# Kernel optimization log

Hardware: AMD Instinct MI355X
Metric: run time of the kernel (lower is better)

Reference implementation:

```python
import jax, jax.numpy as jnp
import numpy as np


def _rel_coords_log(ws: int) -> np.ndarray:
    # matches torch.meshgrid default indexing='ij'
    idx = np.arange(ws, dtype=np.float32)
    coords = np.stack(np.meshgrid(idx, idx, indexing='ij'), axis=0).reshape(2, -1)  # [2, ws^2]
    rel = coords[:, :, None] - coords[:, None, :]  # [2, T, T]
    rel = rel.transpose(1, 2, 0).reshape(-1, 2)    # [T*T, 2]
    return np.sign(rel) * np.log1p(np.abs(rel))


def setup_inputs() -> dict:
    key = jax.random.key(0)
    ks = jax.random.split(key, 9)
    B, C, Hd, ws, meta_h = 256, 256, 8, 16, 256
    s = 1.0 / np.sqrt(C)
    return {
        'x': jax.random.normal(ks[0], (B, C, ws, ws), dtype=jnp.float32),
        'w_qkv': jax.random.normal(ks[1], (3 * C, C), dtype=jnp.float32) * s,
        'b_qkv': jax.random.normal(ks[2], (3 * C,), dtype=jnp.float32) * 0.01,
        'w_proj': jax.random.normal(ks[3], (C, C), dtype=jnp.float32) * s,
        'b_proj': jax.random.normal(ks[4], (C,), dtype=jnp.float32) * 0.01,
        'mw1': jax.random.normal(ks[5], (meta_h, 2), dtype=jnp.float32) * 0.5,
        'mb1': jax.random.normal(ks[6], (meta_h,), dtype=jnp.float32) * 0.01,
        'mw2': jax.random.normal(ks[7], (Hd, meta_h), dtype=jnp.float32) * (1.0 / np.sqrt(meta_h)),
        'mb2': jax.random.normal(ks[8], (Hd,), dtype=jnp.float32) * 0.01,
        'tau': jnp.ones((1, Hd, 1, 1), dtype=jnp.float32),
    }


def reference(x, w_qkv, b_qkv, w_proj, b_proj, mw1, mb1, mw2, mb2, tau):
    B, C, H, W = x.shape
    T = H * W
    nh = tau.shape[1]
    hd = C // nh
    # [B, C, H, W] -> [B, T, C]
    xt = x.reshape(B, C, T).transpose(0, 2, 1)
    qkv = xt @ w_qkv.T + b_qkv                                  # [B, T, 3C]
    qkv = qkv.reshape(B, T, 3, nh, hd).transpose(2, 0, 3, 1, 4)  # [3, B, nh, T, hd]
    q, k, v = qkv[0], qkv[1], qkv[2]
    # cosine similarity attention
    qn = jnp.linalg.norm(q, axis=-1, keepdims=True)              # [B, nh, T, 1]
    kn = jnp.linalg.norm(k, axis=-1, keepdims=True)
    denom = jnp.maximum(qn * kn.transpose(0, 1, 3, 2), 1e-6)
    scores = jnp.einsum('bhqd,bhkd->bhqk', q, k) / denom
    scores = scores / jnp.maximum(tau, 0.01)
    # MLP relative position bias (static coords)
    rc = jnp.asarray(_rel_coords_log(H))                          # [T*T, 2]
    bias = jax.nn.relu(rc @ mw1.T + mb1) @ mw2.T + mb2            # [T*T, nh]
    bias = bias.T.reshape(nh, T, T)
    scores = scores + bias[None]
    attn = jax.nn.softmax(scores, axis=-1)
    out = jnp.einsum('bhqk,bhkd->bhqd', attn, v)                  # [B, nh, T, hd]
    out = out.transpose(0, 2, 1, 3).reshape(B, T, C)
    out = out @ w_proj.T + b_proj
    return out.transpose(0, 2, 1).reshape(B, C, H, W)
```

## Files before the change

kernel.cpp:

```cpp
#include <hip/hip_runtime.h>
#include <math.h>

#define Cc 256
#define NH 8
#define HD 32
#define Tt 256
#define MH 256
#define TBL 961

typedef _Float16 f16;
typedef f16 f16x4 __attribute__((ext_vector_type(4)));
typedef f16 f16x8 __attribute__((ext_vector_type(8)));
typedef float f32x4 __attribute__((ext_vector_type(4)));

__device__ __forceinline__ f16x8 ld8(const f16* base, int row, int kc) {
  return *(const f16x8*)&base[row * 32 + ((kc ^ ((row >> 2) & 3)) << 3)];
}
__device__ __forceinline__ void st8(f16* base, int row, int kc, f16x8 v) {
  *(f16x8*)&base[row * 32 + ((kc ^ ((row >> 2) & 3)) << 3)] = v;
}
__device__ __forceinline__ int sidx(int row, int col) {
  return row * 32 + (((col >> 3) ^ ((row >> 2) & 3)) << 3) + (col & 7);
}
__device__ __forceinline__ int vsidx(int d, int t) {
  return d * 256 + (((t >> 3) ^ (d & 7)) << 3) + (t & 7);
}
__device__ __forceinline__ f16x8 vld8(const f16* base, int d, int tch) {
  return *(const f16x8*)&base[d * 256 + ((tch ^ (d & 7)) << 3)];
}

__global__ __launch_bounds__(256) void prep_kernel(
    const float* __restrict__ mw1, const float* __restrict__ mb1,
    const float* __restrict__ mw2, const float* __restrict__ mb2,
    const float* __restrict__ w_proj, float* __restrict__ table,
    float* __restrict__ tablemax, f16* __restrict__ wpf) {
  int blk = blockIdx.x, tid = threadIdx.x;
  if (blk >= NH) {
    int base = (blk - NH) * 2048 + tid * 8;
    f16x8 v;
#pragma unroll
    for (int u = 0; u < 8; u++) v[u] = (f16)w_proj[base + u];
    *(f16x8*)&wpf[base] = v;
    return;
  }
  __shared__ float s_w1a[MH], s_w1b[MH], s_b1[MH], s_w2[MH];
  __shared__ float red[256];
  for (int i = tid; i < MH; i += 256) {
    s_w1a[i] = mw1[2 * i];
    s_w1b[i] = mw1[2 * i + 1];
    s_b1[i] = mb1[i];
    s_w2[i] = mw2[blk * MH + i];
  }
  __syncthreads();
  float lmax = -1e30f;
  float b2 = mb2[blk];
  for (int idx = tid; idx < TBL; idx += 256) {
    float fdi = (float)(idx / 31 - 15);
    float fdj = (float)(idx % 31 - 15);
    float d0 = (fdi > 0.f ? 1.f : (fdi < 0.f ? -1.f : 0.f)) * log1pf(fabsf(fdi));
    float d1 = (fdj > 0.f ? 1.f : (fdj < 0.f ? -1.f : 0.f)) * log1pf(fabsf(fdj));
    float o = b2;
    for (int m = 0; m < MH; m++) {
      float hid = fmaxf(fmaf(d0, s_w1a[m], fmaf(d1, s_w1b[m], s_b1[m])), 0.f);
      o = fmaf(hid, s_w2[m], o);
    }
    table[blk * TBL + idx] = o;
    lmax = fmaxf(lmax, o);
  }
  red[tid] = lmax;
  __syncthreads();
  for (int s = 128; s > 0; s >>= 1) {
    if (tid < s) red[tid] = fmaxf(red[tid], red[tid + s]);
    __syncthreads();
  }
  if (tid == 0) tablemax[blk] = red[0];
}

__global__ __launch_bounds__(512, 4) void fused_attn(
    const float* __restrict__ x, const float* __restrict__ w_qkv,
    const float* __restrict__ b_qkv, const float* __restrict__ table,
    const float* __restrict__ tablemax, const float* __restrict__ tau,
    f16* __restrict__ attnH) {
  __shared__ __align__(16) char smem[68352];
  f16* Qa = (f16*)smem;
  f16* Ka = (f16*)(smem + 16384);
  f16* Vt = (f16*)(smem + 32768);
  f16* Pspare = (f16*)(smem + 49152);
  float* tbv = (float*)(smem + 51456);
  float* rs = (float*)(smem + 67328);
  f16* Xa = (f16*)smem;
  f16* Wa = (f16*)(smem + 16384);

  int tid = threadIdx.x;
  int o = blockIdx.x;
  int bh = ((o & 7) << 8) | (o >> 3);
  int b = bh >> 3, h = bh & 7;
  int wv = tid >> 6, ln = tid & 63, lq = ln >> 4, lm = ln & 15;

  const float LOG2E = 1.4426950408889634f;
  float rtau = 1.0f / fmaxf(tau[h], 0.01f);
  float tmaxh = tablemax[h];

  for (int idx = tid; idx < 31 * 32; idx += 512) {
    int di_ = idx >> 5, c = idx & 31;
    float4 v;
    float* vp = (float*)&v;
#pragma unroll
    for (int u = 0; u < 4; u++) {
      int dj = c - u;
      dj = dj < 0 ? 0 : (dj > 30 ? 30 : dj);
      vp[u] = (table[h * TBL + di_ * 31 + dj] - tmaxh - rtau * 1.0001f) * LOG2E;
    }
    *(float4*)&tbv[idx * 4] = v;
  }

  float bj[6];
#pragma unroll
  for (int nt = 0; nt < 6; nt++) {
    int n = nt * 16 + lm;
    int row = ((n >> 5) << 8) + (h << 5) + (n & 31);
    bj[nt] = b_qkv[row];
  }

  f32x4 acc[2][6] = {};
  for (int c0 = 0; c0 < Cc; c0 += 32) {
    {
      int t = tid & 255, cg = tid >> 8;
      f16x8 v0, v1;
#pragma unroll
      for (int cc = 0; cc < 8; cc++)
        v0[cc] = (f16)x[(size_t)b * 65536 + (size_t)(c0 + cg * 16 + cc) * 256 + t];
#pragma unroll
      for (int cc = 0; cc < 8; cc++)
        v1[cc] = (f16)x[(size_t)b * 65536 + (size_t)(c0 + cg * 16 + 8 + cc) * 256 + t];
      st8(Xa, t, cg * 2 + 0, v0);
      st8(Xa, t, cg * 2 + 1, v1);
    }
    if (tid < 384) {
      int n = tid >> 2, ck = tid & 3;
      int row = ((n >> 5) << 8) + (h << 5) + (n & 31);
      const float* wp = w_qkv + (size_t)row * Cc + c0 + ck * 8;
      f16x8 v;
#pragma unroll
      for (int u = 0; u < 8; u++) v[u] = (f16)wp[u];
      st8(Wa, n, ck, v);
    }
    __syncthreads();
    f16x8 af[2], bf[6];
#pragma unroll
    for (int e = 0; e < 2; e++) af[e] = ld8(Xa, wv * 32 + e * 16 + lm, lq);
#pragma unroll
    for (int nt = 0; nt < 6; nt++) bf[nt] = ld8(Wa, nt * 16 + lm, lq);
#pragma unroll
    for (int e = 0; e < 2; e++)
#pragma unroll
      for (int nt = 0; nt < 6; nt++)
        acc[e][nt] = __builtin_amdgcn_mfma_f32_16x16x32_f16(af[e], bf[nt],
                                                            acc[e][nt], 0, 0, 0);
    __syncthreads();
  }

#pragma unroll
  for (int e = 0; e < 2; e++) {
#pragma unroll
    for (int nt = 0; nt < 6; nt++) {
      int d = (nt & 1) * 16 + lm;
#pragma unroll
      for (int r = 0; r < 4; r++) {
        int t = wv * 32 + e * 16 + lq * 4 + r;
        f16 v = (f16)(acc[e][nt][r] + bj[nt]);
        if (nt < 2)      Qa[sidx(t, d)] = v;
        else if (nt < 4) Ka[sidx(t, d)] = v;
        else             Vt[vsidx(d, t)] = v;
      }
    }
  }
  __syncthreads();

  if (tid < 256) {
    int t = tid;
    float s = 0.f;
    f16x8 v[4];
#pragma unroll
    for (int ck = 0; ck < 4; ck++) {
      v[ck] = *(f16x8*)&Qa[t * 32 + ck * 8];
#pragma unroll
      for (int u = 0; u < 8; u++) { float f = (float)v[ck][u]; s = fmaf(f, f, s); }
    }
    float sc_ = rsqrtf(s) * rtau * LOG2E;
#pragma unroll
    for (int ck = 0; ck < 4; ck++) {
      f16x8 o2;
#pragma unroll
      for (int u = 0; u < 8; u++) o2[u] = (f16)((float)v[ck][u] * sc_);
      *(f16x8*)&Qa[t * 32 + ck * 8] = o2;
    }
  } else {
    int t = tid - 256;
    float s = 0.f;
    f16x8 v[4];
#pragma unroll
    for (int ck = 0; ck < 4; ck++) {
      v[ck] = *(f16x8*)&Ka[t * 32 + ck * 8];
#pragma unroll
      for (int u = 0; u < 8; u++) { float f = (float)v[ck][u]; s = fmaf(f, f, s); }
    }
    float sc_ = rsqrtf(s);
#pragma unroll
    for (int ck = 0; ck < 4; ck++) {
      f16x8 o2;
#pragma unroll
      for (int u = 0; u < 8; u++) o2[u] = (f16)((float)v[ck][u] * sc_);
      *(f16x8*)&Ka[t * 32 + ck * 8] = o2;
    }
  }
  __syncthreads();

  f16x8 qf[2];
#pragma unroll
  for (int e = 0; e < 2; e++) qf[e] = ld8(Qa, wv * 32 + e * 16 + lm, lq);
  __syncthreads();

  f16* Pme = (wv < 7) ? (Qa + wv * 1152) : Pspare;
  int c0l = lm - lq * 4 + 15;
  const float4* tbp = (const float4*)tbv;
  float lsum[2] = {0.f, 0.f};
  f32x4 acco[2][2] = {};
  int dibase = wv * 2 + 15;

  for (int n0 = 0; n0 < Tt; n0 += 32) {
    f16x8 kf[2];
#pragma unroll
    for (int nt = 0; nt < 2; nt++) kf[nt] = ld8(Ka, n0 + nt * 16 + lm, lq);
    f32x4 zero = {0.f, 0.f, 0.f, 0.f};
    f32x4 sc[2][2];
#pragma unroll
    for (int e = 0; e < 2; e++)
#pragma unroll
      for (int nt = 0; nt < 2; nt++)
        sc[e][nt] = __builtin_amdgcn_mfma_f32_16x16x32_f16(kf[nt], qf[e], zero,
                                                           0, 0, 0);
#pragma unroll
    for (int e = 0; e < 2; e++) {
#pragma unroll
      for (int nt = 0; nt < 2; nt++) {
        int di_ = dibase + e - (n0 >> 4) - nt;
        float4 bv = tbp[di_ * 32 + c0l];
        const float* bvp = (const float*)&bv;
        f16x4 pv;
#pragma unroll
        for (int r = 0; r < 4; r++) {
          float p = exp2f(sc[e][nt][r] + bvp[r]);
          lsum[e] += p;
          pv[r] = (f16)p;
        }
        *(f16x4*)&Pme[(e * 16 + lm) * 36 + nt * 16 + lq * 4] = pv;
      }
    }
    asm volatile("s_waitcnt lgkmcnt(0)" ::: "memory");
    f16x8 pf[2], vf[2];
#pragma unroll
    for (int e = 0; e < 2; e++) {
      f16x4 p0 = *(f16x4*)&Pme[(e * 16 + lm) * 36 + lq * 8];
      f16x4 p1 = *(f16x4*)&Pme[(e * 16 + lm) * 36 + lq * 8 + 4];
      pf[e] = __builtin_shufflevector(p0, p1, 0, 1, 2, 3, 4, 5, 6, 7);
    }
#pragma unroll
    for (int dt = 0; dt < 2; dt++)
      vf[dt] = vld8(Vt, dt * 16 + lm, (n0 >> 3) + lq);
#pragma unroll
    for (int e = 0; e < 2; e++)
#pragma unroll
      for (int dt = 0; dt < 2; dt++)
        acco[e][dt] = __builtin_amdgcn_mfma_f32_16x16x32_f16(pf[e], vf[dt],
                                                             acco[e][dt], 0, 0, 0);
  }

#pragma unroll
  for (int e = 0; e < 2; e++) {
    float v = lsum[e];
    v += __shfl_xor(v, 16);
    v += __shfl_xor(v, 32);
    lsum[e] = v;
  }
  if (ln < 16) {
    rs[wv * 32 + lm] = lsum[0];
    rs[wv * 32 + 16 + lm] = lsum[1];
  }
  asm volatile("s_waitcnt lgkmcnt(0)" ::: "memory");
#pragma unroll
  for (int e = 0; e < 2; e++)
#pragma unroll
    for (int r = 0; r < 4; r++) {
      float rl = __builtin_amdgcn_rcpf(rs[wv * 32 + e * 16 + lq * 4 + r]);
      int q = wv * 32 + e * 16 + lq * 4 + r;
#pragma unroll
      for (int dt = 0; dt < 2; dt++) {
        int d = dt * 16 + lm;
        attnH[((size_t)b * Tt + q) * Cc + h * HD + d] =
            (f16)(acco[e][dt][r] * rl);
      }
    }
}

__global__ __launch_bounds__(256, 4) void proj_gemm(
    const f16* __restrict__ A, const f16* __restrict__ wf,
    const float* __restrict__ bp, float* __restrict__ out) {
  __shared__ __align__(16) f16 Af[128 * 72];
  __shared__ __align__(16) f16 Wsh[128 * 72];
  __shared__ float sB[128];
  int tid = threadIdx.x;
  int row0 = blockIdx.x * 128;
  int n0g = blockIdx.y * 128;
  int b = row0 >> 8, t0 = row0 & 255;
  int wv = tid >> 6, ln = tid & 63, lq = ln >> 4, lm = ln & 15;
  int cw = (wv & 1) * 64, tw = (wv >> 1) * 64;

  if (tid < 128) sB[tid] = bp[n0g + tid];

  f32x4 acc[4][4] = {};
  for (int k0 = 0; k0 < Cc; k0 += 64) {
#pragma unroll
    for (int p = 0; p < 4; p++) {
      int idx = p * 256 + tid;
      int row = idx >> 3, ch = idx & 7;
      f16x8 v = *(const f16x8*)&A[(size_t)(row0 + row) * Cc + k0 + ch * 8];
      *(f16x8*)&Af[row * 72 + ch * 8] = v;
    }
#pragma unroll
    for (int p = 0; p < 4; p++) {
      int idx = p * 256 + tid;
      int row = idx >> 3, ch = idx & 7;
      f16x8 v = *(const f16x8*)&wf[(size_t)(n0g + row) * Cc + k0 + ch * 8];
      *(f16x8*)&Wsh[row * 72 + ch * 8] = v;
    }
    __syncthreads();
#pragma unroll
    for (int kk = 0; kk < 2; kk++) {
      f16x8 wfr[4], af[4];
#pragma unroll
      for (int i = 0; i < 4; i++)
        wfr[i] = *(f16x8*)&Wsh[(cw + i * 16 + lm) * 72 + (kk * 4 + lq) * 8];
#pragma unroll
      for (int j = 0; j < 4; j++)
        af[j] = *(f16x8*)&Af[(tw + j * 16 + lm) * 72 + (kk * 4 + lq) * 8];
#pragma unroll
      for (int i = 0; i < 4; i++)
#pragma unroll
        for (int j = 0; j < 4; j++)
          acc[i][j] = __builtin_amdgcn_mfma_f32_16x16x32_f16(wfr[i], af[j],
                                                             acc[i][j], 0, 0, 0);
    }
    __syncthreads();
  }

#pragma unroll
  for (int i = 0; i < 4; i++)
#pragma unroll
    for (int r = 0; r < 4; r++) {
      int crl = cw + i * 16 + lq * 4 + r;
      float bias = sB[crl];
#pragma unroll
      for (int j = 0; j < 4; j++) {
        int tcl = tw + j * 16 + lm;
        out[(size_t)b * 65536 + (size_t)(n0g + crl) * 256 + t0 + tcl] =
            acc[i][j][r] + bias;
      }
    }
}

extern "C" void kernel_launch(void* const* d_in, const int* in_sizes, int n_in,
                              void* d_out, int out_size, void* d_ws,
                              size_t ws_size, hipStream_t stream) {
  const float* x = (const float*)d_in[0];
  const float* w_qkv = (const float*)d_in[1];
  const float* b_qkv = (const float*)d_in[2];
  const float* w_proj = (const float*)d_in[3];
  const float* b_proj = (const float*)d_in[4];
  const float* mw1 = (const float*)d_in[5];
  const float* mb1 = (const float*)d_in[6];
  const float* mw2 = (const float*)d_in[7];
  const float* mb2 = (const float*)d_in[8];
  const float* tau = (const float*)d_in[9];
  float* out = (float*)d_out;

  const size_t NEEDED = (size_t)(TBL * NH + NH) * 4 + (size_t)65536 * 2 +
                        (size_t)256 * NH * Tt * HD * 2;
  if (ws_size < NEEDED) return;

  float* table = (float*)d_ws;
  float* tablemax = table + TBL * NH;
  f16* wpf = (f16*)(tablemax + NH);
  f16* attnH = wpf + 65536;

  prep_kernel<<<40, 256, 0, stream>>>(mw1, mb1, mw2, mb2, w_proj, table,
                                      tablemax, wpf);
  fused_attn<<<256 * NH, 512, 0, stream>>>(x, w_qkv, b_qkv, table, tablemax,
                                           tau, attnH);
  dim3 g3(512, 2);
  proj_gemm<<<g3, 256, 0, stream>>>(attnH, wpf, b_proj, out);
}
```

Measured before the change: 265.0 us.

## Pre-transpose x and pre-convert w_qkv to fp16 with prefetched staging

Adds a transpose kernel that converts x into a token-major fp16 layout, and extends the prep kernel to convert w_qkv into a per-head-reordered fp16 copy. Both scratch buffers live in the output buffer, which is only written later. The attention kernel now loads contiguous 16-byte fp16 vectors instead of strided fp32 scalars, and it register-prefetches the next k-chunk while the current one is consumed. The eight heads of each batch no longer each re-read and convert x from fp32. The cost is an extra kernel launch, an extra pass over x, and reuse of the output buffer as scratch.

```diff
diff --git a/kernel.cpp b/kernel.cpp
--- a/kernel.cpp
+++ b/kernel.cpp
@@ -32,9 +32,26 @@
 __global__ __launch_bounds__(256) void prep_kernel(
     const float* __restrict__ mw1, const float* __restrict__ mb1,
     const float* __restrict__ mw2, const float* __restrict__ mb2,
-    const float* __restrict__ w_proj, float* __restrict__ table,
-    float* __restrict__ tablemax, f16* __restrict__ wpf) {
+    const float* __restrict__ w_proj, const float* __restrict__ w_qkv,
+    float* __restrict__ table, float* __restrict__ tablemax,
+    f16* __restrict__ wpf, f16* __restrict__ wqf) {
   int blk = blockIdx.x, tid = threadIdx.x;
+  if (blk >= NH + 32) {
+    int blk2 = blk - NH - 32;
+#pragma unroll
+    for (int pass = 0; pass < 4; pass++) {
+      int chunkid = blk2 * 256 + tid + pass * 6144;
+      int row = chunkid >> 5, ck = chunkid & 31;
+      int hh = row / 96, n = row % 96;
+      int srow = ((n >> 5) << 8) + (hh << 5) + (n & 31);
+      const float* wp = w_qkv + (size_t)srow * Cc + ck * 8;
+      f16x8 v;
+#pragma unroll
+      for (int u = 0; u < 8; u++) v[u] = (f16)wp[u];
+      *(f16x8*)&wqf[(size_t)row * Cc + ck * 8] = v;
+    }
+    return;
+  }
   if (blk >= NH) {
     int base = (blk - NH) * 2048 + tid * 8;
     f16x8 v;
@@ -76,8 +93,33 @@
   if (tid == 0) tablemax[blk] = red[0];
 }
 
+__global__ __launch_bounds__(256) void xpose_kernel(const float* __restrict__ x,
+                                                    f16* __restrict__ xt) {
+  __shared__ __align__(16) f16 tile[64 * 72];
+  int blk = blockIdx.x;
+  int b = blk >> 4, ti = (blk >> 2) & 3, tj = blk & 3;
+  int tid = threadIdx.x;
+  int tl = tid & 63, cg = tid >> 6;
+  const float* xb = x + (size_t)b * 65536;
+#pragma unroll
+  for (int u = 0; u < 16; u++) {
+    int cl = cg * 16 + u;
+    float v = xb[(size_t)(ti * 64 + cl) * 256 + tj * 64 + tl];
+    tile[tl * 72 + (((cl >> 3) ^ (tl & 7)) << 3) + (cl & 7)] = (f16)v;
+  }
+  __syncthreads();
+  f16* xtb = xt + (size_t)b * 65536;
+#pragma unroll
+  for (int u = 0; u < 2; u++) {
+    int chunk = tid * 2 + u;
+    int tr = chunk >> 3, ck = chunk & 7;
+    f16x8 v = *(const f16x8*)&tile[tr * 72 + ((ck ^ (tr & 7)) << 3)];
+    *(f16x8*)&xtb[(size_t)(tj * 64 + tr) * 256 + ti * 64 + ck * 8] = v;
+  }
+}
+
 __global__ __launch_bounds__(512, 4) void fused_attn(
-    const float* __restrict__ x, const float* __restrict__ w_qkv,
+    const f16* __restrict__ xt, const f16* __restrict__ wqf,
     const float* __restrict__ b_qkv, const float* __restrict__ table,
     const float* __restrict__ tablemax, const float* __restrict__ tau,
     f16* __restrict__ attnH) {
@@ -122,30 +164,27 @@
     bj[nt] = b_qkv[row];
   }
 
+  const f16* xtb = xt + (size_t)b * 65536;
+  const f16* wqh = wqf + (size_t)h * 24576;
+  int xt_ = tid >> 1, xkc = (tid & 1) * 2;
+  int wn = tid >> 2, wck = tid & 3;
+
   f32x4 acc[2][6] = {};
+  f16x8 xv0, xv1, wvv;
+  xv0 = *(const f16x8*)&xtb[xt_ * 256 + xkc * 8];
+  xv1 = *(const f16x8*)&xtb[xt_ * 256 + xkc * 8 + 8];
+  if (tid < 384) wvv = *(const f16x8*)&wqh[wn * 256 + wck * 8];
+
   for (int c0 = 0; c0 < Cc; c0 += 32) {
-    {
-      int t = tid & 255, cg = tid >> 8;
-      f16x8 v0, v1;
-#pragma unroll
-      for (int cc = 0; cc < 8; cc++)
-        v0[cc] = (f16)x[(size_t)b * 65536 + (size_t)(c0 + cg * 16 + cc) * 256 + t];
-#pragma unroll
-      for (int cc = 0; cc < 8; cc++)
-        v1[cc] = (f16)x[(size_t)b * 65536 + (size_t)(c0 + cg * 16 + 8 + cc) * 256 + t];
-      st8(Xa, t, cg * 2 + 0, v0);
-      st8(Xa, t, cg * 2 + 1, v1);
-    }
-    if (tid < 384) {
-      int n = tid >> 2, ck = tid & 3;
-      int row = ((n >> 5) << 8) + (h << 5) + (n & 31);
-      const float* wp = w_qkv + (size_t)row * Cc + c0 + ck * 8;
-      f16x8 v;
-#pragma unroll
-      for (int u = 0; u < 8; u++) v[u] = (f16)wp[u];
-      st8(Wa, n, ck, v);
-    }
+    st8(Xa, xt_, xkc, xv0);
+    st8(Xa, xt_, xkc + 1, xv1);
+    if (tid < 384) st8(Wa, wn, wck, wvv);
     __syncthreads();
+    if (c0 + 32 < Cc) {
+      xv0 = *(const f16x8*)&xtb[xt_ * 256 + c0 + 32 + xkc * 8];
+      xv1 = *(const f16x8*)&xtb[xt_ * 256 + c0 + 32 + xkc * 8 + 8];
+      if (tid < 384) wvv = *(const f16x8*)&wqh[wn * 256 + c0 + 32 + wck * 8];
+    }
     f16x8 af[2], bf[6];
 #pragma unroll
     for (int e = 0; e < 2; e++) af[e] = ld8(Xa, wv * 32 + e * 16 + lm, lq);
@@ -393,9 +432,13 @@
   f16* wpf = (f16*)(tablemax + NH);
   f16* attnH = wpf + 65536;
 
-  prep_kernel<<<40, 256, 0, stream>>>(mw1, mb1, mw2, mb2, w_proj, table,
-                                      tablemax, wpf);
-  fused_attn<<<256 * NH, 512, 0, stream>>>(x, w_qkv, b_qkv, table, tablemax,
+  f16* xt = (f16*)d_out;
+  f16* wqf = (f16*)d_out + (size_t)256 * 65536;
+
+  prep_kernel<<<64, 256, 0, stream>>>(mw1, mb1, mw2, mb2, w_proj, w_qkv, table,
+                                      tablemax, wpf, wqf);
+  xpose_kernel<<<4096, 256, 0, stream>>>(x, xt);
+  fused_attn<<<256 * NH, 512, 0, stream>>>(xt, wqf, b_qkv, table, tablemax,
                                            tau, attnH);
   dim3 g3(512, 2);
   proj_gemm<<<g3, 256, 0, stream>>>(attnH, wpf, b_proj, out);
```

Measured after the change: 257.2 us. -3.0%, faster.
